# Performance work log

Measured on AMD Instinct MI355X. Metric: run time of the kernel, lower is better.

## Reference

```python
import jax, jax.numpy as jnp
import numpy as np

HIDDEN = 512


def _lstm(x, kernel, rec, bias):
    # x: [B,T,D]; Keras gate order i,f,c(g),o
    xz = jnp.einsum('btd,dk->btk', x, kernel) + bias  # [B,T,4H]
    B = x.shape[0]
    init = (jnp.zeros((B, HIDDEN), x.dtype), jnp.zeros((B, HIDDEN), x.dtype))

    def step(carry, z_t):
        h, c = carry
        z = z_t + h @ rec
        i, f, g, o = jnp.split(z, 4, axis=-1)
        c = jax.nn.sigmoid(f) * c + jax.nn.sigmoid(i) * jnp.tanh(g)
        h = jax.nn.sigmoid(o) * jnp.tanh(c)
        return (h, c), h

    _, hs = jax.lax.scan(step, init, jnp.swapaxes(xz, 0, 1))
    return jnp.swapaxes(hs, 0, 1)  # [B,T,H]


def _bilstm(x, kf, rf, bf, kb, rb, bb):
    fwd = _lstm(x, kf, rf, bf)
    bwd = _lstm(x[:, ::-1], kb, rb, bb)[:, ::-1]
    return jnp.concatenate([fwd, bwd], axis=-1)  # [B,T,2H]


def _crf_nll(logits, tags, seq_lens, trans):
    # logits [B,T,N], tags [B,T] int, seq_lens [B] int, trans [N,N]
    B, T, N = logits.shape
    t_idx = jnp.arange(T)
    mask = (t_idx[None, :] < seq_lens[:, None])  # [B,T] bool
    maskf = mask.astype(logits.dtype)

    # gold sequence score: unary + pairwise transitions
    unary = jnp.take_along_axis(logits, tags[..., None], axis=-1)[..., 0]  # [B,T]
    unary_score = jnp.sum(unary * maskf, axis=-1)
    pair_maskf = maskf[:, 1:]  # pair (t-1,t) valid iff t < len
    binary = trans[tags[:, :-1], tags[:, 1:]]  # [B,T-1]
    binary_score = jnp.sum(binary * pair_maskf, axis=-1)

    # log-partition via forward algorithm (masked scan)
    alpha0 = logits[:, 0]  # [B,N]

    def step(alpha, inp):
        logit_t, valid = inp
        new = jax.nn.logsumexp(alpha[:, :, None] + trans[None], axis=1) + logit_t
        return jnp.where(valid[:, None], new, alpha), None

    xs = (jnp.swapaxes(logits[:, 1:], 0, 1), jnp.swapaxes(mask[:, 1:], 0, 1))
    alpha, _ = jax.lax.scan(step, alpha0, xs)
    log_z = jax.nn.logsumexp(alpha, axis=-1)  # [B]
    return -(unary_score + binary_score - log_z)


def setup_inputs() -> dict:
    key = jax.random.key(0)
    ks = jax.random.split(key, 12)
    B, T, D, H, N = 32, 256, 768, HIDDEN, 25
    s_in = 1.0 / np.sqrt(D)
    s_rec = 1.0 / np.sqrt(H)
    return {
        'embeddings': jax.random.normal(ks[0], (B, T, D), jnp.float32),
        'targets': jax.random.randint(ks[1], (B, T), 0, N, jnp.int32),
        'seq_lens': jax.random.randint(ks[2], (B,), 1, T + 1, jnp.int32),
        'k_fwd': jax.random.normal(ks[3], (D, 4 * H), jnp.float32) * s_in,
        'r_fwd': jax.random.normal(ks[4], (H, 4 * H), jnp.float32) * s_rec,
        'b_fwd': jnp.zeros((4 * H,), jnp.float32),
        'k_bwd': jax.random.normal(ks[5], (D, 4 * H), jnp.float32) * s_in,
        'r_bwd': jax.random.normal(ks[6], (H, 4 * H), jnp.float32) * s_rec,
        'b_bwd': jnp.zeros((4 * H,), jnp.float32),
        'dense_w': jax.random.normal(ks[7], (2 * H, N), jnp.float32) / np.sqrt(2 * H),
        'dense_b': jnp.zeros((N,), jnp.float32),
        'transitions': jax.random.uniform(ks[8], (N, N), jnp.float32),
    }


def reference(embeddings, targets, seq_lens, k_fwd, r_fwd, b_fwd,
              k_bwd, r_bwd, b_bwd, dense_w, dense_b, transitions):
    seq_lens = jnp.clip(seq_lens, 1, embeddings.shape[1])
    h = _bilstm(embeddings, k_fwd, r_fwd, b_fwd, k_bwd, r_bwd, b_bwd)
    logits = jax.nn.selu(jnp.einsum('bth,hn->btn', h, dense_w) + dense_b)
    nll = _crf_nll(logits, targets, seq_lens, transitions)  # [B]
    loss = jnp.mean(nll)
    return loss, logits
```

## Files before the change

kernel.cpp:

```cpp
#include <hip/hip_runtime.h>
#include <hip/hip_bf16.h>
#include <math.h>

#define HID 512
#define GATES 2048
#define BT 8192
#define TT 256
#define BB 32
#define DIN 768
#define NTAG 25
#define UPB 4
#define NBLK 128
#define FSTR 4
#define EREP 8
#define ESTR 16

typedef _Float16 half2v __attribute__((ext_vector_type(2)));
typedef _Float16 half8  __attribute__((ext_vector_type(8)));
typedef float    f32x4  __attribute__((ext_vector_type(4)));

__device__ __forceinline__ half2v pack2h(float a, float b) {
  return __builtin_bit_cast(half2v, __builtin_amdgcn_cvt_pkrtz(a, b));
}

__device__ __forceinline__ float sigf(float x) { return 1.f / (1.f + __expf(-x)); }

__device__ __forceinline__ void gld_lds16(const void* g, void* l) {
  __builtin_amdgcn_global_load_lds(
      (const __attribute__((address_space(1))) unsigned int*)g,
      (__attribute__((address_space(3))) unsigned int*)l, 16, 0, 0);
}

__global__ __launch_bounds__(256) void prep_all(
    const float* __restrict__ emb, unsigned short* __restrict__ emb16,
    const float* __restrict__ Kf, const float* __restrict__ Kb,
    unsigned short* __restrict__ KTf, unsigned short* __restrict__ KTb,
    const float* __restrict__ W, unsigned short* __restrict__ WT16)
{
  __shared__ float tile[64][65];
  const int bid = blockIdx.x;
  const int tid = threadIdx.x;

  if (bid < 1024) {
    const int m = bid * 8 + (tid >> 5);
    const int c0 = tid & 31;
    #pragma unroll
    for (int p = 0; p < 3; ++p) {
      const int c = c0 + p * 32;
      const int kb = c >> 3, s = c & 7;
      const float* src = emb + (size_t)m * DIN + c * 8;
      const float4 v0 = *(const float4*)src;
      const float4 v1 = *(const float4*)(src + 4);
      half8 hv;
      hv[0] = (_Float16)v0.x; hv[1] = (_Float16)v0.y;
      hv[2] = (_Float16)v0.z; hv[3] = (_Float16)v0.w;
      hv[4] = (_Float16)v1.x; hv[5] = (_Float16)v1.y;
      hv[6] = (_Float16)v1.z; hv[7] = (_Float16)v1.w;
      *(half8*)(emb16 + (size_t)m * DIN + kb * 64 + (s ^ (m & 7)) * 8) = hv;
    }
  } else if (bid < 1792) {
    const int r = bid - 1024;
    const int dir = r / 384;
    const int r2 = r % 384;
    const int k0 = (r2 >> 5) * 64;
    const int n0 = (r2 & 31) * 64;
    const float* __restrict__ K = dir ? Kb : Kf;
    unsigned short* __restrict__ KT = dir ? KTb : KTf;
    #pragma unroll
    for (int p = 0; p < 4; ++p) {
      const int idx = p * 256 + tid;
      const int kr = idx >> 4, c4 = (idx & 15) * 4;
      const float4 v = *(const float4*)(K + (size_t)(k0 + kr) * GATES + n0 + c4);
      tile[kr][c4 + 0] = v.x; tile[kr][c4 + 1] = v.y;
      tile[kr][c4 + 2] = v.z; tile[kr][c4 + 3] = v.w;
    }
    __syncthreads();
    #pragma unroll
    for (int p = 0; p < 2; ++p) {
      const int idx = p * 256 + tid;
      const int nr = idx >> 3, s = idx & 7;
      half8 hv;
      #pragma unroll
      for (int x = 0; x < 8; ++x) hv[x] = (_Float16)tile[s * 8 + x][nr];
      *(half8*)(KT + (size_t)(n0 + nr) * DIN + k0 + (s ^ (nr & 7)) * 8) = hv;
    }
  } else {
    for (int id = tid; id < 32 * 1024; id += 256) {
      const int n = id >> 10, k = id & 1023;
      const float v = (n < NTAG) ? W[(size_t)k * NTAG + n] : 0.f;
      ((_Float16*)WT16)[id] = (_Float16)v;
    }
  }
}

__global__ __launch_bounds__(256) void gemm_xz(
    const unsigned short* __restrict__ emb16,
    const unsigned short* __restrict__ KTf, const unsigned short* __restrict__ KTb,
    const float* __restrict__ bf, const float* __restrict__ bb,
    _Float16* __restrict__ xzf, _Float16* __restrict__ xzb)
{
  const int dir = blockIdx.z;
  const unsigned short* __restrict__ KT = dir ? KTb : KTf;
  const float* __restrict__ bias = dir ? bb : bf;
  _Float16* __restrict__ C = dir ? xzb : xzf;
  const int n0 = blockIdx.x * 128;
  const int m0 = blockIdx.y * 128;

  __shared__ __align__(16) char A_lds[128 * 64 * 2];
  __shared__ __align__(16) char B_lds[128 * 64 * 2];

  const int tid = threadIdx.x;
  const int lane = tid & 63, wid = tid >> 6;
  const int wm = wid >> 1, wn = wid & 1;
  const int lm = lane & 15, lk = lane >> 4;

  f32x4 acc[4][4];
  #pragma unroll
  for (int i = 0; i < 4; ++i)
    #pragma unroll
    for (int j = 0; j < 4; ++j) acc[i][j] = (f32x4){0.f, 0.f, 0.f, 0.f};

  for (int kt = 0; kt < DIN / 64; ++kt) {
    __syncthreads();
    #pragma unroll
    for (int i = 0; i < 4; ++i) {
      const int g = wid * 256 + i * 64 + lane;
      const int r = g >> 3, s = g & 7;
      gld_lds16(emb16 + (size_t)(m0 + r) * DIN + (kt * 8 + s) * 8,
                A_lds + (size_t)(wid * 256 + i * 64) * 16);
      gld_lds16(KT + (size_t)(n0 + r) * DIN + (kt * 8 + s) * 8,
                B_lds + (size_t)(wid * 256 + i * 64) * 16);
    }
    __syncthreads();

    #pragma unroll
    for (int kh = 0; kh < 2; ++kh) {
      half8 a[4], b[4];
      #pragma unroll
      for (int mt = 0; mt < 4; ++mt) {
        const int rloc = wm * 64 + mt * 16 + lm;
        const int kslot = kh * 4 + lk;
        a[mt] = *(const half8*)(A_lds + rloc * 128 + ((kslot ^ (rloc & 7)) << 4));
      }
      #pragma unroll
      for (int nt = 0; nt < 4; ++nt) {
        const int nloc = wn * 64 + nt * 16 + lm;
        const int kslot = kh * 4 + lk;
        b[nt] = *(const half8*)(B_lds + nloc * 128 + ((kslot ^ (nloc & 7)) << 4));
      }
      #pragma unroll
      for (int mt = 0; mt < 4; ++mt)
        #pragma unroll
        for (int nt = 0; nt < 4; ++nt)
          acc[mt][nt] = __builtin_amdgcn_mfma_f32_16x16x32_f16(a[mt], b[nt], acc[mt][nt], 0, 0, 0);
    }
  }

  #pragma unroll
  for (int nt = 0; nt < 4; ++nt) {
    const int col = n0 + wn * 64 + nt * 16 + lm;
    const float bs = bias[col];
    #pragma unroll
    for (int mt = 0; mt < 4; ++mt) {
      const int rowb = m0 + wm * 64 + mt * 16 + lk * 4;
      const f32x4 v = acc[mt][nt];
      #pragma unroll
      for (int g = 0; g < 4; ++g)
        C[(size_t)(rowb + g) * GATES + col] = (_Float16)(v[g] + bs);
    }
  }
}

__global__ __launch_bounds__(256, 1) void lstm_persist(
    const _Float16* __restrict__ xzf, const _Float16* __restrict__ xzb,
    const float* __restrict__ Rf, const float* __restrict__ Rb,
    unsigned int* __restrict__ hGf, unsigned int* __restrict__ hGb,
    int* __restrict__ flg,
    int* __restrict__ ep)
{
  const int bid = blockIdx.x;
  const int dir = bid & 1;
  const int blk = bid >> 1;
  const int u0 = blk * UPB;
  const int tid = threadIdx.x;
  const int c = tid & 15;
  const int j = (c & 3) * HID + u0 + (c >> 2);
  const int lane = tid & 63, w = tid >> 6;
  const int lm = lane & 15, lk = lane >> 4;

  const float* __restrict__ R  = dir ? Rb : Rf;
  const _Float16* __restrict__ xz = dir ? xzb : xzf;
  unsigned int* __restrict__ hGd = dir ? hGb : hGf;
  int* __restrict__ flgd = flg + (size_t)dir * TT * NBLK * FSTR;
  int* __restrict__ epd  = ep  + (size_t)dir * TT * EREP * ESTR;

  __shared__ uint4 hs4[4 * 32 * 17];
  __shared__ float redm[4][BB][18];

  half8 Rbf[4];
  #pragma unroll
  for (int kti = 0; kti < 4; ++kti) {
    const int kb = (w * 4 + kti) * 32 + lk * 8;
    half8 hv;
    #pragma unroll
    for (int x = 0; x < 8; ++x) hv[x] = (_Float16)R[(size_t)(kb + x) * GATES + j];
    Rbf[kti] = hv;
  }

  float cst = 0.f;
  const int b_o = tid & 31, u_o = tid >> 5;
  uint4* myhs = hs4 + w * (32 * 17);
  const int sr = lane >> 4, si = lane & 15;
  const bool leader = (blk == 0);

  for (int s = 0; s < TT; ++s) {
    const int t = dir ? (TT - 1 - s) : s;

    float xg[4] = {0.f, 0.f, 0.f, 0.f};
    if (tid < 128) {
      #pragma unroll
      for (int g = 0; g < 4; ++g)
        xg[g] = (float)xz[((size_t)b_o * TT + t) * GATES + g * HID + u0 + u_o];
    }

    if (s > 0) {
      const int tprev = dir ? t + 1 : t - 1;
      if (leader) {
        if (tid < NBLK) {
          while (!__hip_atomic_load(&flgd[((s - 1) * NBLK + tid) * FSTR],
                                    __ATOMIC_RELAXED, __HIP_MEMORY_SCOPE_AGENT))
            __builtin_amdgcn_s_sleep(1);
        }
        __syncthreads();
        if (tid < EREP)
          __hip_atomic_store(&epd[((s - 1) * EREP + tid) * ESTR], 1,
                             __ATOMIC_RELAXED, __HIP_MEMORY_SCOPE_AGENT);
      } else {
        if (tid == 0) {
          while (!__hip_atomic_load(&epd[((s - 1) * EREP + (blk & 7)) * ESTR],
                                    __ATOMIC_RELAXED, __HIP_MEMORY_SCOPE_AGENT))
            __builtin_amdgcn_s_sleep(1);
        }
        __syncthreads();
      }
      const uint4* hsrc = (const uint4*)(hGd + (size_t)tprev * BB * 256);
      #pragma unroll
      for (int it = 0; it < 8; ++it) {
        const int r = it * 4 + sr;
        myhs[r * 17 + si] = hsrc[r * 64 + w * 16 + si];
      }
    } else {
      const uint4 zz = make_uint4(0u, 0u, 0u, 0u);
      #pragma unroll
      for (int it = 0; it < 8; ++it) {
        const int r = it * 4 + sr;
        myhs[r * 17 + si] = zz;
      }
    }

    f32x4 acc0 = (f32x4){0.f, 0.f, 0.f, 0.f};
    f32x4 acc1 = (f32x4){0.f, 0.f, 0.f, 0.f};
    #pragma unroll
    for (int kti = 0; kti < 4; ++kti) {
      const int cidx = kti * 4 + lk;
      const half8 a0 = *(const half8*)&myhs[lm * 17 + cidx];
      const half8 a1 = *(const half8*)&myhs[(16 + lm) * 17 + cidx];
      acc0 = __builtin_amdgcn_mfma_f32_16x16x32_f16(a0, Rbf[kti], acc0, 0, 0, 0);
      acc1 = __builtin_amdgcn_mfma_f32_16x16x32_f16(a1, Rbf[kti], acc1, 0, 0, 0);
    }
    #pragma unroll
    for (int g = 0; g < 4; ++g) {
      redm[w][lk * 4 + g][lm] = acc0[g];
      redm[w][16 + lk * 4 + g][lm] = acc1[g];
    }
    __syncthreads();

    if (tid < 128) {
      float z[4];
      #pragma unroll
      for (int g = 0; g < 4; ++g) {
        const int cc = u_o * 4 + g;
        z[g] = redm[0][b_o][cc] + redm[1][b_o][cc] + redm[2][b_o][cc] +
               redm[3][b_o][cc] + xg[g];
      }
      cst = sigf(z[1]) * cst + sigf(z[0]) * tanhf(z[2]);
      const float h = sigf(z[3]) * tanhf(cst);
      const float hp2 = __shfl_xor(h, 32);
      if ((tid & 32) == 0) {
        const half2v p = pack2h(h, hp2);
        __hip_atomic_store(&hGd[((size_t)t * BB + b_o) * 256 + blk * 2 + (u_o >> 1)],
                           __builtin_bit_cast(unsigned int, p),
                           __ATOMIC_RELAXED, __HIP_MEMORY_SCOPE_AGENT);
      }
    }
    __syncthreads();
    if (tid == 0)
      __hip_atomic_store(&flgd[(s * NBLK + blk) * FSTR], 1, __ATOMIC_RELAXED,
                         __HIP_MEMORY_SCOPE_AGENT);
  }
}

__global__ __launch_bounds__(256) void dense_selu(
    const unsigned int* __restrict__ hGf, const unsigned int* __restrict__ hGb,
    const unsigned short* __restrict__ WT16, const float* __restrict__ bias,
    float* __restrict__ out, float* __restrict__ loss0)
{
  if (blockIdx.x == 0 && threadIdx.x == 0) *loss0 = 0.f;
  const int q0 = blockIdx.x * 128;
  __shared__ __align__(16) char A_lds[128 * 64 * 2];
  __shared__ __align__(16) char B_lds[32 * 64 * 2];

  const int tid = threadIdx.x;
  const int lane = tid & 63, w = tid >> 6;
  const int lm = lane & 15, lk = lane >> 4;

  f32x4 acc[2][2];
  #pragma unroll
  for (int i = 0; i < 2; ++i)
    #pragma unroll
    for (int jj = 0; jj < 2; ++jj) acc[i][jj] = (f32x4){0.f, 0.f, 0.f, 0.f};

  for (int kt = 0; kt < 16; ++kt) {
    const int k0 = kt * 64;
    __syncthreads();
    #pragma unroll
    for (int p = 0; p < 4; ++p) {
      const int id = p * 256 + tid;
      const int r = id >> 3, s = id & 7;
      const int k = k0 + s * 8;
      const unsigned int* src = (k < 512)
          ? hGf + (size_t)(q0 + r) * 256 + (k >> 1)
          : hGb + (size_t)(q0 + r) * 256 + ((k - 512) >> 1);
      const uint4 v = *(const uint4*)src;
      *(uint4*)(A_lds + r * 128 + ((s ^ (r & 7)) << 4)) = v;
    }
    {
      const int r = tid >> 3, s = tid & 7;
      const uint4 v = *(const uint4*)(WT16 + (size_t)r * 1024 + k0 + s * 8);
      *(uint4*)(B_lds + r * 128 + ((s ^ (r & 7)) << 4)) = v;
    }
    __syncthreads();

    #pragma unroll
    for (int kh = 0; kh < 2; ++kh) {
      const int kslot = kh * 4 + lk;
      half8 a[2], b[2];
      #pragma unroll
      for (int mt = 0; mt < 2; ++mt) {
        const int rloc = w * 32 + mt * 16 + lm;
        a[mt] = *(const half8*)(A_lds + rloc * 128 + ((kslot ^ (rloc & 7)) << 4));
      }
      #pragma unroll
      for (int nt = 0; nt < 2; ++nt) {
        const int nloc = nt * 16 + lm;
        b[nt] = *(const half8*)(B_lds + nloc * 128 + ((kslot ^ (nloc & 7)) << 4));
      }
      #pragma unroll
      for (int mt = 0; mt < 2; ++mt)
        #pragma unroll
        for (int nt = 0; nt < 2; ++nt)
          acc[mt][nt] = __builtin_amdgcn_mfma_f32_16x16x32_f16(a[mt], b[nt], acc[mt][nt], 0, 0, 0);
    }
  }

  const float scale = 1.0507009873554805f, alf = 1.6732632423543772f;
  #pragma unroll
  for (int nt = 0; nt < 2; ++nt) {
    const int col = nt * 16 + lm;
    if (col < NTAG) {
      const float bs = bias[col];
      #pragma unroll
      for (int mt = 0; mt < 2; ++mt) {
        const int rowb = q0 + w * 32 + mt * 16 + lk * 4;
        const f32x4 vv = acc[mt][nt];
        #pragma unroll
        for (int g = 0; g < 4; ++g) {
          const int q = rowb + g;
          const int bt = (q & 31) * 256 + (q >> 5);
          float v = vv[g] + bs;
          v = v > 0.f ? scale * v : scale * alf * (__expf(v) - 1.f);
          out[(size_t)bt * NTAG + col] = v;
        }
      }
    }
  }
}

__global__ __launch_bounds__(64) void crf_kernel(
    const float* __restrict__ logits,
    const int* __restrict__ tags, const int* __restrict__ lens,
    const float* __restrict__ trans, float* __restrict__ loss0)
{
  const int b = blockIdx.x;
  const int tid = threadIdx.x;
  __shared__ float tr[NTAG * NTAG];
  __shared__ float al[NTAG];
  __shared__ float red[2];
  for (int i = tid; i < NTAG * NTAG; i += 64) tr[i] = trans[i];
  __syncthreads();

  int len = lens[b];
  len = len < 1 ? 1 : (len > TT ? TT : len);
  const size_t base = (size_t)b * TT;

  float us = 0.f, bs = 0.f;
  for (int t = tid; t < TT; t += 64) {
    if (t < len) us += logits[(base + t) * NTAG + tags[base + t]];
    if (t >= 1 && t < len) bs += tr[tags[base + t - 1] * NTAG + tags[base + t]];
  }
  #pragma unroll
  for (int off = 32; off > 0; off >>= 1) {
    us += __shfl_down(us, off);
    bs += __shfl_down(bs, off);
  }
  if (tid == 0) { red[0] = us; red[1] = bs; }

  if (tid < NTAG) al[tid] = logits[base * NTAG + tid];
  __syncthreads();

  for (int t = 1; t < len; ++t) {
    float nv = 0.f;
    if (tid < NTAG) {
      float m = -3.4e38f;
      #pragma unroll
      for (int i = 0; i < NTAG; ++i) m = fmaxf(m, al[i] + tr[i * NTAG + tid]);
      float ss = 0.f;
      #pragma unroll
      for (int i = 0; i < NTAG; ++i) ss += __expf(al[i] + tr[i * NTAG + tid] - m);
      nv = m + __logf(ss) + logits[(base + t) * NTAG + tid];
    }
    __syncthreads();
    if (tid < NTAG) al[tid] = nv;
    __syncthreads();
  }

  if (tid == 0) {
    float m = -3.4e38f;
    for (int i = 0; i < NTAG; ++i) m = fmaxf(m, al[i]);
    float ss = 0.f;
    for (int i = 0; i < NTAG; ++i) ss += __expf(al[i] - m);
    const float logz = m + __logf(ss);
    const float nll = -(red[0] + red[1] - logz);
    atomicAdd(loss0, nll * (1.f / BB));
  }
}

extern "C" void kernel_launch(void* const* d_in, const int* in_sizes, int n_in,
                              void* d_out, int out_size, void* d_ws, size_t ws_size,
                              hipStream_t stream) {
  const float* emb  = (const float*)d_in[0];
  const int* tags   = (const int*)d_in[1];
  const int* lens   = (const int*)d_in[2];
  const float* kf   = (const float*)d_in[3];
  const float* rf   = (const float*)d_in[4];
  const float* bf   = (const float*)d_in[5];
  const float* kb   = (const float*)d_in[6];
  const float* rb   = (const float*)d_in[7];
  const float* bb   = (const float*)d_in[8];
  const float* dw   = (const float*)d_in[9];
  const float* db   = (const float*)d_in[10];
  const float* trans= (const float*)d_in[11];
  float* out = (float*)d_out;

  _Float16* xzf = (_Float16*)d_ws;
  _Float16* xzb = xzf + (size_t)BT * GATES;
  unsigned int* hGf = (unsigned int*)(xzb + (size_t)BT * GATES);
  unsigned int* hGb = hGf + (size_t)TT * BB * 256;
  unsigned short* emb16 = (unsigned short*)(hGb + (size_t)TT * BB * 256);
  unsigned short* KTf = emb16 + (size_t)BT * DIN;
  unsigned short* KTb = KTf + (size_t)GATES * DIN;
  unsigned short* WT16 = KTb + (size_t)GATES * DIN;
  int* flg = (int*)(WT16 + 32 * 1024);
  int* ep  = flg + 2 * TT * NBLK * FSTR;

  (void)hipMemsetAsync(flg, 0,
                       (size_t)(2 * TT * NBLK * FSTR + 2 * TT * EREP * ESTR) * 4,
                       stream);

  prep_all<<<1793, 256, 0, stream>>>(emb, emb16, kf, kb, KTf, KTb, dw, WT16);
  gemm_xz<<<dim3(GATES / 128, BT / 128, 2), 256, 0, stream>>>(emb16, KTf, KTb, bf, bb, xzf, xzb);
  lstm_persist<<<2 * NBLK, 256, 0, stream>>>(xzf, xzb, rf, rb, hGf, hGb, flg, ep);
  dense_selu<<<BT / 128, 256, 0, stream>>>(hGf, hGb, WT16, db, out + 1, out);
  crf_kernel<<<32, 64, 0, stream>>>(out + 1, tags, lens, trans, out);
}
```

Baseline: 893.5 us.

## Fuse input projection GEMM into persistent LSTM kernel with register-resident K slices

Removes the separate input-projection GEMM and the fp16 xz buffer. Each persistent LSTM block now keeps its slice of the input kernel in registers and computes x_t·K per step with MFMA, reading a time-major fp16 copy of the embeddings. This drops the GEMM launch, the K transpose prep and the round trip of the xz intermediate through memory. In exchange it adds per-step embedding loads and six extra MFMAs per wave inside the serial recurrence, plus more register pressure. Those loads do not depend on h, so they may overlap with the wait for the previous step.

New measurement: 1.057 ms. +18.3%, slower.

```diff
diff --git a/kernel.cpp b/kernel.cpp
--- a/kernel.cpp
+++ b/kernel.cpp
@@ -25,29 +25,19 @@
 
 __device__ __forceinline__ float sigf(float x) { return 1.f / (1.f + __expf(-x)); }
 
-__device__ __forceinline__ void gld_lds16(const void* g, void* l) {
-  __builtin_amdgcn_global_load_lds(
-      (const __attribute__((address_space(1))) unsigned int*)g,
-      (__attribute__((address_space(3))) unsigned int*)l, 16, 0, 0);
-}
-
 __global__ __launch_bounds__(256) void prep_all(
     const float* __restrict__ emb, unsigned short* __restrict__ emb16,
-    const float* __restrict__ Kf, const float* __restrict__ Kb,
-    unsigned short* __restrict__ KTf, unsigned short* __restrict__ KTb,
     const float* __restrict__ W, unsigned short* __restrict__ WT16)
 {
-  __shared__ float tile[64][65];
   const int bid = blockIdx.x;
   const int tid = threadIdx.x;
-
   if (bid < 1024) {
     const int m = bid * 8 + (tid >> 5);
+    const int b = m >> 8, t = m & 255;
     const int c0 = tid & 31;
     #pragma unroll
     for (int p = 0; p < 3; ++p) {
       const int c = c0 + p * 32;
-      const int kb = c >> 3, s = c & 7;
       const float* src = emb + (size_t)m * DIN + c * 8;
       const float4 v0 = *(const float4*)src;
       const float4 v1 = *(const float4*)(src + 4);
@@ -56,33 +46,7 @@
       hv[2] = (_Float16)v0.z; hv[3] = (_Float16)v0.w;
       hv[4] = (_Float16)v1.x; hv[5] = (_Float16)v1.y;
       hv[6] = (_Float16)v1.z; hv[7] = (_Float16)v1.w;
-      *(half8*)(emb16 + (size_t)m * DIN + kb * 64 + (s ^ (m & 7)) * 8) = hv;
-    }
-  } else if (bid < 1792) {
-    const int r = bid - 1024;
-    const int dir = r / 384;
-    const int r2 = r % 384;
-    const int k0 = (r2 >> 5) * 64;
-    const int n0 = (r2 & 31) * 64;
-    const float* __restrict__ K = dir ? Kb : Kf;
-    unsigned short* __restrict__ KT = dir ? KTb : KTf;
-    #pragma unroll
-    for (int p = 0; p < 4; ++p) {
-      const int idx = p * 256 + tid;
-      const int kr = idx >> 4, c4 = (idx & 15) * 4;
-      const float4 v = *(const float4*)(K + (size_t)(k0 + kr) * GATES + n0 + c4);
-      tile[kr][c4 + 0] = v.x; tile[kr][c4 + 1] = v.y;
-      tile[kr][c4 + 2] = v.z; tile[kr][c4 + 3] = v.w;
-    }
-    __syncthreads();
-    #pragma unroll
-    for (int p = 0; p < 2; ++p) {
-      const int idx = p * 256 + tid;
-      const int nr = idx >> 3, s = idx & 7;
-      half8 hv;
-      #pragma unroll
-      for (int x = 0; x < 8; ++x) hv[x] = (_Float16)tile[s * 8 + x][nr];
-      *(half8*)(KT + (size_t)(n0 + nr) * DIN + k0 + (s ^ (nr & 7)) * 8) = hv;
+      *(half8*)(emb16 + ((size_t)t * BB + b) * DIN + c * 8) = hv;
     }
   } else {
     for (int id = tid; id < 32 * 1024; id += 256) {
@@ -93,87 +57,11 @@
   }
 }
 
-__global__ __launch_bounds__(256) void gemm_xz(
+__global__ __launch_bounds__(256, 1) void lstm_persist(
     const unsigned short* __restrict__ emb16,
-    const unsigned short* __restrict__ KTf, const unsigned short* __restrict__ KTb,
+    const float* __restrict__ Kf, const float* __restrict__ Kb,
+    const float* __restrict__ Rf, const float* __restrict__ Rb,
     const float* __restrict__ bf, const float* __restrict__ bb,
-    _Float16* __restrict__ xzf, _Float16* __restrict__ xzb)
-{
-  const int dir = blockIdx.z;
-  const unsigned short* __restrict__ KT = dir ? KTb : KTf;
-  const float* __restrict__ bias = dir ? bb : bf;
-  _Float16* __restrict__ C = dir ? xzb : xzf;
-  const int n0 = blockIdx.x * 128;
-  const int m0 = blockIdx.y * 128;
-
-  __shared__ __align__(16) char A_lds[128 * 64 * 2];
-  __shared__ __align__(16) char B_lds[128 * 64 * 2];
-
-  const int tid = threadIdx.x;
-  const int lane = tid & 63, wid = tid >> 6;
-  const int wm = wid >> 1, wn = wid & 1;
-  const int lm = lane & 15, lk = lane >> 4;
-
-  f32x4 acc[4][4];
-  #pragma unroll
-  for (int i = 0; i < 4; ++i)
-    #pragma unroll
-    for (int j = 0; j < 4; ++j) acc[i][j] = (f32x4){0.f, 0.f, 0.f, 0.f};
-
-  for (int kt = 0; kt < DIN / 64; ++kt) {
-    __syncthreads();
-    #pragma unroll
-    for (int i = 0; i < 4; ++i) {
-      const int g = wid * 256 + i * 64 + lane;
-      const int r = g >> 3, s = g & 7;
-      gld_lds16(emb16 + (size_t)(m0 + r) * DIN + (kt * 8 + s) * 8,
-                A_lds + (size_t)(wid * 256 + i * 64) * 16);
-      gld_lds16(KT + (size_t)(n0 + r) * DIN + (kt * 8 + s) * 8,
-                B_lds + (size_t)(wid * 256 + i * 64) * 16);
-    }
-    __syncthreads();
-
-    #pragma unroll
-    for (int kh = 0; kh < 2; ++kh) {
-      half8 a[4], b[4];
-      #pragma unroll
-      for (int mt = 0; mt < 4; ++mt) {
-        const int rloc = wm * 64 + mt * 16 + lm;
-        const int kslot = kh * 4 + lk;
-        a[mt] = *(const half8*)(A_lds + rloc * 128 + ((kslot ^ (rloc & 7)) << 4));
-      }
-      #pragma unroll
-      for (int nt = 0; nt < 4; ++nt) {
-        const int nloc = wn * 64 + nt * 16 + lm;
-        const int kslot = kh * 4 + lk;
-        b[nt] = *(const half8*)(B_lds + nloc * 128 + ((kslot ^ (nloc & 7)) << 4));
-      }
-      #pragma unroll
-      for (int mt = 0; mt < 4; ++mt)
-        #pragma unroll
-        for (int nt = 0; nt < 4; ++nt)
-          acc[mt][nt] = __builtin_amdgcn_mfma_f32_16x16x32_f16(a[mt], b[nt], acc[mt][nt], 0, 0, 0);
-    }
-  }
-
-  #pragma unroll
-  for (int nt = 0; nt < 4; ++nt) {
-    const int col = n0 + wn * 64 + nt * 16 + lm;
-    const float bs = bias[col];
-    #pragma unroll
-    for (int mt = 0; mt < 4; ++mt) {
-      const int rowb = m0 + wm * 64 + mt * 16 + lk * 4;
-      const f32x4 v = acc[mt][nt];
-      #pragma unroll
-      for (int g = 0; g < 4; ++g)
-        C[(size_t)(rowb + g) * GATES + col] = (_Float16)(v[g] + bs);
-    }
-  }
-}
-
-__global__ __launch_bounds__(256, 1) void lstm_persist(
-    const _Float16* __restrict__ xzf, const _Float16* __restrict__ xzb,
-    const float* __restrict__ Rf, const float* __restrict__ Rb,
     unsigned int* __restrict__ hGf, unsigned int* __restrict__ hGb,
     int* __restrict__ flg,
     int* __restrict__ ep)
@@ -188,8 +76,9 @@
   const int lane = tid & 63, w = tid >> 6;
   const int lm = lane & 15, lk = lane >> 4;
 
+  const float* __restrict__ K  = dir ? Kb : Kf;
   const float* __restrict__ R  = dir ? Rb : Rf;
-  const _Float16* __restrict__ xz = dir ? xzb : xzf;
+  const float* __restrict__ bias = dir ? bb : bf;
   unsigned int* __restrict__ hGd = dir ? hGb : hGf;
   int* __restrict__ flgd = flg + (size_t)dir * TT * NBLK * FSTR;
   int* __restrict__ epd  = ep  + (size_t)dir * TT * EREP * ESTR;
@@ -206,9 +95,23 @@
     for (int x = 0; x < 8; ++x) hv[x] = (_Float16)R[(size_t)(kb + x) * GATES + j];
     Rbf[kti] = hv;
   }
+  half8 Kbf[6];
+  #pragma unroll
+  for (int kt = 0; kt < 6; ++kt) {
+    const int kb = w * 192 + kt * 32 + lk * 8;
+    half8 hv;
+    #pragma unroll
+    for (int x = 0; x < 8; ++x) hv[x] = (_Float16)K[(size_t)(kb + x) * GATES + j];
+    Kbf[kt] = hv;
+  }
 
   float cst = 0.f;
   const int b_o = tid & 31, u_o = tid >> 5;
+  float bg[4] = {0.f, 0.f, 0.f, 0.f};
+  if (tid < 128) {
+    #pragma unroll
+    for (int g = 0; g < 4; ++g) bg[g] = bias[g * HID + u0 + u_o];
+  }
   uint4* myhs = hs4 + w * (32 * 17);
   const int sr = lane >> 4, si = lane & 15;
   const bool leader = (blk == 0);
@@ -216,11 +119,22 @@
   for (int s = 0; s < TT; ++s) {
     const int t = dir ? (TT - 1 - s) : s;
 
-    float xg[4] = {0.f, 0.f, 0.f, 0.f};
-    if (tid < 128) {
-      #pragma unroll
-      for (int g = 0; g < 4; ++g)
-        xg[g] = (float)xz[((size_t)b_o * TT + t) * GATES + g * HID + u0 + u_o];
+    const uint4* erow = (const uint4*)(emb16 + (size_t)t * BB * DIN);
+    uint4 e0[6], e1[6];
+    #pragma unroll
+    for (int kt = 0; kt < 6; ++kt) {
+      const int ci = w * 24 + kt * 4 + lk;
+      e0[kt] = erow[lm * 96 + ci];
+      e1[kt] = erow[(16 + lm) * 96 + ci];
+    }
+    f32x4 acc0 = (f32x4){0.f, 0.f, 0.f, 0.f};
+    f32x4 acc1 = (f32x4){0.f, 0.f, 0.f, 0.f};
+    #pragma unroll
+    for (int kt = 0; kt < 6; ++kt) {
+      acc0 = __builtin_amdgcn_mfma_f32_16x16x32_f16(
+          __builtin_bit_cast(half8, e0[kt]), Kbf[kt], acc0, 0, 0, 0);
+      acc1 = __builtin_amdgcn_mfma_f32_16x16x32_f16(
+          __builtin_bit_cast(half8, e1[kt]), Kbf[kt], acc1, 0, 0, 0);
     }
 
     if (s > 0) {
@@ -249,25 +163,16 @@
         const int r = it * 4 + sr;
         myhs[r * 17 + si] = hsrc[r * 64 + w * 16 + si];
       }
-    } else {
-      const uint4 zz = make_uint4(0u, 0u, 0u, 0u);
-      #pragma unroll
-      for (int it = 0; it < 8; ++it) {
-        const int r = it * 4 + sr;
-        myhs[r * 17 + si] = zz;
-      }
-    }
-
-    f32x4 acc0 = (f32x4){0.f, 0.f, 0.f, 0.f};
-    f32x4 acc1 = (f32x4){0.f, 0.f, 0.f, 0.f};
-    #pragma unroll
-    for (int kti = 0; kti < 4; ++kti) {
-      const int cidx = kti * 4 + lk;
-      const half8 a0 = *(const half8*)&myhs[lm * 17 + cidx];
-      const half8 a1 = *(const half8*)&myhs[(16 + lm) * 17 + cidx];
-      acc0 = __builtin_amdgcn_mfma_f32_16x16x32_f16(a0, Rbf[kti], acc0, 0, 0, 0);
-      acc1 = __builtin_amdgcn_mfma_f32_16x16x32_f16(a1, Rbf[kti], acc1, 0, 0, 0);
-    }
+      #pragma unroll
+      for (int kti = 0; kti < 4; ++kti) {
+        const int cidx = kti * 4 + lk;
+        const half8 a0 = *(const half8*)&myhs[lm * 17 + cidx];
+        const half8 a1 = *(const half8*)&myhs[(16 + lm) * 17 + cidx];
+        acc0 = __builtin_amdgcn_mfma_f32_16x16x32_f16(a0, Rbf[kti], acc0, 0, 0, 0);
+        acc1 = __builtin_amdgcn_mfma_f32_16x16x32_f16(a1, Rbf[kti], acc1, 0, 0, 0);
+      }
+    }
+
     #pragma unroll
     for (int g = 0; g < 4; ++g) {
       redm[w][lk * 4 + g][lm] = acc0[g];
@@ -281,7 +186,7 @@
       for (int g = 0; g < 4; ++g) {
         const int cc = u_o * 4 + g;
         z[g] = redm[0][b_o][cc] + redm[1][b_o][cc] + redm[2][b_o][cc] +
-               redm[3][b_o][cc] + xg[g];
+               redm[3][b_o][cc] + bg[g];
       }
       cst = sigf(z[1]) * cst + sigf(z[0]) * tanhf(z[2]);
       const float h = sigf(z[3]) * tanhf(cst);
@@ -462,14 +367,10 @@
   const float* trans= (const float*)d_in[11];
   float* out = (float*)d_out;
 
-  _Float16* xzf = (_Float16*)d_ws;
-  _Float16* xzb = xzf + (size_t)BT * GATES;
-  unsigned int* hGf = (unsigned int*)(xzb + (size_t)BT * GATES);
+  unsigned int* hGf = (unsigned int*)d_ws;
   unsigned int* hGb = hGf + (size_t)TT * BB * 256;
   unsigned short* emb16 = (unsigned short*)(hGb + (size_t)TT * BB * 256);
-  unsigned short* KTf = emb16 + (size_t)BT * DIN;
-  unsigned short* KTb = KTf + (size_t)GATES * DIN;
-  unsigned short* WT16 = KTb + (size_t)GATES * DIN;
+  unsigned short* WT16 = emb16 + (size_t)BT * DIN;
   int* flg = (int*)(WT16 + 32 * 1024);
   int* ep  = flg + 2 * TT * NBLK * FSTR;
 
@@ -477,9 +378,9 @@
                        (size_t)(2 * TT * NBLK * FSTR + 2 * TT * EREP * ESTR) * 4,
                        stream);
 
-  prep_all<<<1793, 256, 0, stream>>>(emb, emb16, kf, kb, KTf, KTb, dw, WT16);
-  gemm_xz<<<dim3(GATES / 128, BT / 128, 2), 256, 0, stream>>>(emb16, KTf, KTb, bf, bb, xzf, xzb);
-  lstm_persist<<<2 * NBLK, 256, 0, stream>>>(xzf, xzb, rf, rb, hGf, hGb, flg, ep);
+  prep_all<<<1025, 256, 0, stream>>>(emb, emb16, dw, WT16);
+  lstm_persist<<<2 * NBLK, 256, 0, stream>>>(emb16, kf, kb, rf, rb, bf, bb,
+                                             hGf, hGb, flg, ep);
   dense_selu<<<BT / 128, 256, 0, stream>>>(hGf, hGb, WT16, db, out + 1, out);
   crf_kernel<<<32, 64, 0, stream>>>(out + 1, tags, lens, trans, out);
 }
```
